# Kernel optimization log

Measured on AMD Instinct MI355X. Metric: run time of the kernel, lower is better.

Reference implementation:

```python
import jax, jax.numpy as jnp
import numpy as np

B, D_IN, D_HID, D_OUT = 32768, 512, 4096, 512
EPS = 1e-12  # F.normalize eps


def setup_inputs() -> dict:
    key = jax.random.key(0)
    ks = jax.random.split(key, 9)
    # Weights scaled up from the original 0.001 init so the norm_max clamp
    # branch is actually exercised (norms vary around the threshold).
    return {
        "x": jax.random.normal(ks[0], (B, D_IN), jnp.float32),
        "in_mean": jax.random.normal(ks[1], (D_IN,), jnp.float32) * 0.1,
        "in_std": jax.random.uniform(ks[2], (D_IN,), jnp.float32, 0.5, 1.5),
        "out_mean": jax.random.normal(ks[3], (D_OUT,), jnp.float32) * 0.1,
        "out_std": jax.random.uniform(ks[4], (D_OUT,), jnp.float32, 0.5, 1.5),
        "W1": jax.random.normal(ks[5], (D_HID, D_IN), jnp.float32) * 0.02,
        "b1": jax.random.normal(ks[6], (D_HID,), jnp.float32) * 0.001,
        "W2": jax.random.normal(ks[7], (D_OUT, D_HID), jnp.float32) * 0.02,
        "b2": jax.random.normal(ks[8], (D_OUT,), jnp.float32) * 0.001,
        "norm_max": 1,
    }


def reference(x, in_mean, in_std, out_mean, out_std, W1, b1, W2, b2, norm_max):
    norm_max = jnp.float32(norm_max)
    x_copy = x[..., :512]
    # input normalization
    xn = (x - in_mean) / in_std
    # 2-layer MLP: Linear -> ReLU -> Linear
    h = jax.nn.relu(jnp.einsum("bi,hi->bh", xn, W1) + b1)
    res = jnp.einsum("bh,oh->bo", h, W2) + b2
    # vectorized per-row norm clamp (torch loop: rescale rows with norm > norm_max)
    norms = jnp.linalg.norm(res, axis=-1, keepdims=True)  # [B,1]
    scale = norm_max / jax.lax.stop_gradient(norms)
    res = jnp.where(norms > norm_max, res * scale, res)
    # output de-normalization (torch subtracts norm_input[0] here)
    res = res * out_std + out_mean - in_mean
    # residual + L2 normalize
    mapped = res + x_copy
    mnorm = jnp.linalg.norm(mapped, axis=-1, keepdims=True)
    return mapped / jnp.maximum(mnorm, EPS)
```

## Files before the change

kernel.cpp:

```cpp
#include <hip/hip_runtime.h>
#include <hip/hip_bf16.h>

#define NB 32768
#define DIN 512
#define DHID 4096
#define DOUT 512

typedef __attribute__((ext_vector_type(8))) __bf16 bf16x8;
typedef __attribute__((ext_vector_type(4))) float f32x4;

__device__ __forceinline__ unsigned short f2bf(float f) {
  unsigned u = __builtin_bit_cast(unsigned, f);
  u += 0x7FFFu + ((u >> 16) & 1u);
  return (unsigned short)(u >> 16);
}

__device__ __forceinline__ void gload16(void* lds, const void* g) {
  __builtin_amdgcn_global_load_lds(
      (const __attribute__((address_space(1))) void*)g,
      (__attribute__((address_space(3))) void*)lds, 16, 0, 0);
}

__global__ __launch_bounds__(256) void k_prep_x(
    const float4* __restrict__ x, const float* __restrict__ mean,
    const float* __restrict__ stdv, ushort4* __restrict__ xn) {
  const int i = blockIdx.x * 256 + threadIdx.x;
  const int col = (i << 2) & (DIN - 1);
  const float4 v = x[i];
  const float4 m = *(const float4*)(mean + col);
  const float4 s = *(const float4*)(stdv + col);
  ushort4 o;
  o.x = f2bf((v.x - m.x) / s.x);
  o.y = f2bf((v.y - m.y) / s.y);
  o.z = f2bf((v.z - m.z) / s.z);
  o.w = f2bf((v.w - m.w) / s.w);
  xn[i] = o;
}

__global__ __launch_bounds__(256) void k_cvt(
    const float4* __restrict__ in, ushort4* __restrict__ out) {
  const int i = blockIdx.x * 256 + threadIdx.x;
  const float4 v = in[i];
  ushort4 o;
  o.x = f2bf(v.x); o.y = f2bf(v.y); o.z = f2bf(v.z); o.w = f2bf(v.w);
  out[i] = o;
}

__global__ __launch_bounds__(512, 2) void k_gemm1(
    const unsigned short* __restrict__ A, const unsigned short* __restrict__ W,
    const float* __restrict__ bias, unsigned short* __restrict__ outp,
    const int N, const int K, const int nbn) {
  __shared__ __align__(16) char lds[3 * 49152];
  const int tid = threadIdx.x;
  const int wave = tid >> 6, lane = tid & 63;
  const int wm = wave >> 1, wn = wave & 1;
  const int lidlo = lane & 15, lidhi = lane >> 4;

  const int nwg = (int)gridDim.x;
  const int wg = (int)blockIdx.x;
  const int q = nwg >> 3, r = nwg & 7;
  const int xcd = wg & 7, loc = wg >> 3;
  const int swz = (xcd < r ? xcd * (q + 1) : r * (q + 1) + (xcd - r) * q) + loc;
  const int bm = swz / nbn, bn = swz % nbn;
  const int R0 = bm * 256, C0 = bn * 128;

  const int NT = K >> 6;
  const int dbase0 = wave * 1024;

  auto STAGE = [&](int t, int s) {
    char* as = lds + s * 49152;
    char* bs = as + 32768;
    const int k0 = t << 6;
#pragma unroll
    for (int i = 0; i < 4; ++i) {
      const int db = i * 8192 + dbase0;
      const int d = db + lane * 16;
      const int row = d >> 7;
      const int colb = (d & 127) ^ ((row & 7) << 4);
      gload16(as + db,
              (const char*)A + ((size_t)(R0 + row) * K + k0) * 2 + colb);
    }
#pragma unroll
    for (int i = 0; i < 2; ++i) {
      const int db = i * 8192 + dbase0;
      const int d = db + lane * 16;
      const int row = d >> 7;
      const int colb = (d & 127) ^ ((row & 7) << 4);
      gload16(bs + db,
              (const char*)W + ((size_t)(C0 + row) * K + k0) * 2 + colb);
    }
  };

  f32x4 acc[4][4] = {};

  STAGE(0, 0);
  STAGE(1, 1);
  asm volatile("s_waitcnt vmcnt(6)" ::: "memory");
  __builtin_amdgcn_s_barrier();

  int slot = 0;
  for (int t = 0; t < NT; ++t) {
    const int nslot = (slot == 2) ? 0 : slot + 1;
    const int sslot = (nslot == 2) ? 0 : nslot + 1;
    if (t + 2 < NT) STAGE(t + 2, sslot);

    const char* as = lds + slot * 49152;
    const char* bs = as + 32768;
    bf16x8 af[2][4], bw[2][4];
#pragma unroll
    for (int kk = 0; kk < 2; ++kk) {
#pragma unroll
      for (int i = 0; i < 4; ++i) {
        const int ra = wm * 64 + i * 16 + lidlo;
        af[kk][i] = *(const bf16x8*)(
            as + ra * 128 + ((kk * 64 + lidhi * 16) ^ ((ra & 7) << 4)));
        const int rb = wn * 64 + i * 16 + lidlo;
        bw[kk][i] = *(const bf16x8*)(
            bs + rb * 128 + ((kk * 64 + lidhi * 16) ^ ((rb & 7) << 4)));
      }
    }
    __builtin_amdgcn_s_setprio(1);
#pragma unroll
    for (int kk = 0; kk < 2; ++kk)
#pragma unroll
      for (int i = 0; i < 4; ++i)
#pragma unroll
        for (int j = 0; j < 4; ++j)
          acc[i][j] = __builtin_amdgcn_mfma_f32_16x16x32_bf16(
              af[kk][i], bw[kk][j], acc[i][j], 0, 0, 0);
    __builtin_amdgcn_s_setprio(0);

    if (t + 2 < NT) {
      asm volatile("s_waitcnt vmcnt(6)" ::: "memory");
    } else {
      asm volatile("s_waitcnt vmcnt(0)" ::: "memory");
    }
    __builtin_amdgcn_s_barrier();
    slot = nslot;
  }

  const int m0 = R0 + wm * 64 + (lidhi << 2);
  const int n0 = C0 + wn * 64 + lidlo;
#pragma unroll
  for (int j = 0; j < 4; ++j) {
    const int n = n0 + j * 16;
    const float bv = bias[n];
#pragma unroll
    for (int i = 0; i < 4; ++i) {
#pragma unroll
      for (int rr = 0; rr < 4; ++rr) {
        const int m = m0 + i * 16 + rr;
        float v = fmaxf(acc[i][j][rr] + bv, 0.0f);
        outp[(size_t)m * N + n] = f2bf(v);
      }
    }
  }
}

__global__ __launch_bounds__(512, 2) void k_gemm2(
    const unsigned short* __restrict__ A, const unsigned short* __restrict__ W,
    const float* __restrict__ bias, const float* __restrict__ x,
    const float* __restrict__ out_mean, const float* __restrict__ out_std,
    const float* __restrict__ in_mean, const int* __restrict__ nmp,
    float* __restrict__ outp, const int K) {
  __shared__ __align__(16) char lds[2 * 81920];
  const int tid = threadIdx.x;
  const int wave = tid >> 6, lane = tid & 63;
  const int wm = wave >> 2, wn = wave & 3;
  const int lidlo = lane & 15, lidhi = lane >> 4;

  const int nwg = (int)gridDim.x;
  const int wg = (int)blockIdx.x;
  const int q = nwg >> 3, r = nwg & 7;
  const int xcd = wg & 7, loc = wg >> 3;
  const int bm = (xcd < r ? xcd * (q + 1) : r * (q + 1) + (xcd - r) * q) + loc;
  const int R0 = bm * 128;

  const int NT = K >> 6;

  auto STAGE = [&](int t, int s) {
    char* as = lds + s * 81920;
    char* bs = as + 16384;
    const int k0 = t << 6;
#pragma unroll
    for (int i = 0; i < 10; ++i) {
      const int c = wave * 10 + i;
      if (c < 16) {
        const int d = c * 1024 + lane * 16;
        const int row = d >> 7;
        const int colb = (d & 127) ^ ((row & 7) << 4);
        gload16(as + c * 1024,
                (const char*)A + ((size_t)(R0 + row) * K + k0) * 2 + colb);
      } else {
        const int d = (c - 16) * 1024 + lane * 16;
        const int row = d >> 7;
        const int colb = (d & 127) ^ ((row & 7) << 4);
        gload16(bs + (c - 16) * 1024,
                (const char*)W + ((size_t)row * K + k0) * 2 + colb);
      }
    }
  };

  f32x4 acc[4][8] = {};

  STAGE(0, 0);
  asm volatile("s_waitcnt vmcnt(0)" ::: "memory");
  __builtin_amdgcn_s_barrier();

  for (int t = 0; t < NT; ++t) {
    if (t + 1 < NT) STAGE(t + 1, (t + 1) & 1);
    const char* as = lds + (t & 1) * 81920;
    const char* bs = as + 16384;
#pragma unroll
    for (int kk = 0; kk < 2; ++kk) {
      bf16x8 af[4], bw[8];
#pragma unroll
      for (int i = 0; i < 4; ++i) {
        const int ra = wm * 64 + i * 16 + lidlo;
        af[i] = *(const bf16x8*)(
            as + ra * 128 + ((kk * 64 + lidhi * 16) ^ ((ra & 7) << 4)));
      }
#pragma unroll
      for (int j = 0; j < 8; ++j) {
        const int rb = wn * 128 + j * 16 + lidlo;
        bw[j] = *(const bf16x8*)(
            bs + rb * 128 + ((kk * 64 + lidhi * 16) ^ ((rb & 7) << 4)));
      }
      __builtin_amdgcn_s_setprio(1);
#pragma unroll
      for (int i = 0; i < 4; ++i)
#pragma unroll
        for (int j = 0; j < 8; ++j)
          acc[i][j] = __builtin_amdgcn_mfma_f32_16x16x32_bf16(
              af[i], bw[j], acc[i][j], 0, 0, 0);
      __builtin_amdgcn_s_setprio(0);
    }
    asm volatile("s_waitcnt vmcnt(0)" ::: "memory");
    __builtin_amdgcn_s_barrier();
  }

  float* red = (float*)lds;
  const int n0 = wn * 128 + lidlo;
  float bv[8], os[8], omim[8];
#pragma unroll
  for (int j = 0; j < 8; ++j) {
    const int n = n0 + j * 16;
    bv[j] = bias[n];
    os[j] = out_std[n];
    omim[j] = out_mean[n] - in_mean[n];
  }
  const float nm = (float)(*nmp);
  const int lmb = wm * 64 + (lidhi << 2);

  float scr[4][4];
#pragma unroll
  for (int i = 0; i < 4; ++i) {
#pragma unroll
    for (int rr = 0; rr < 4; ++rr) {
      float s = 0.0f;
#pragma unroll
      for (int j = 0; j < 8; ++j) {
        const float v = acc[i][j][rr] + bv[j];
        acc[i][j][rr] = v;
        s += v * v;
      }
      s += __shfl_xor(s, 1); s += __shfl_xor(s, 2);
      s += __shfl_xor(s, 4); s += __shfl_xor(s, 8);
      scr[i][rr] = s;
    }
  }
  if (lidlo == 0) {
#pragma unroll
    for (int i = 0; i < 4; ++i)
#pragma unroll
      for (int rr = 0; rr < 4; ++rr)
        red[wn * 128 + lmb + i * 16 + rr] = scr[i][rr];
  }
  __syncthreads();
#pragma unroll
  for (int i = 0; i < 4; ++i) {
#pragma unroll
    for (int rr = 0; rr < 4; ++rr) {
      const int lm = lmb + i * 16 + rr;
      const float t = red[lm] + red[128 + lm] + red[256 + lm] + red[384 + lm];
      const float rn = sqrtf(t);
      scr[i][rr] = (rn > nm) ? (nm / rn) : 1.0f;
    }
  }
  __syncthreads();

  float s2a[4][4];
#pragma unroll
  for (int i = 0; i < 4; ++i) {
#pragma unroll
    for (int rr = 0; rr < 4; ++rr) {
      const int row = R0 + lmb + i * 16 + rr;
      const float sc = scr[i][rr];
      float s = 0.0f;
#pragma unroll
      for (int j = 0; j < 8; ++j) {
        const int n = n0 + j * 16;
        const float mv = acc[i][j][rr] * sc * os[j] + omim[j] +
                         x[(size_t)row * DOUT + n];
        acc[i][j][rr] = mv;
        s += mv * mv;
      }
      s += __shfl_xor(s, 1); s += __shfl_xor(s, 2);
      s += __shfl_xor(s, 4); s += __shfl_xor(s, 8);
      s2a[i][rr] = s;
    }
  }
  if (lidlo == 0) {
#pragma unroll
    for (int i = 0; i < 4; ++i)
#pragma unroll
      for (int rr = 0; rr < 4; ++rr)
        red[wn * 128 + lmb + i * 16 + rr] = s2a[i][rr];
  }
  __syncthreads();
#pragma unroll
  for (int i = 0; i < 4; ++i) {
#pragma unroll
    for (int rr = 0; rr < 4; ++rr) {
      const int lm = lmb + i * 16 + rr;
      const float t = red[lm] + red[128 + lm] + red[256 + lm] + red[384 + lm];
      const float inv = 1.0f / fmaxf(sqrtf(t), 1e-12f);
      const int row = R0 + lm;
#pragma unroll
      for (int j = 0; j < 8; ++j) {
        const int n = n0 + j * 16;
        outp[(size_t)row * DOUT + n] = acc[i][j][rr] * inv;
      }
    }
  }
}

extern "C" void kernel_launch(void* const* d_in, const int* in_sizes, int n_in,
                              void* d_out, int out_size, void* d_ws, size_t ws_size,
                              hipStream_t stream) {
  const float* x = (const float*)d_in[0];
  const float* in_mean = (const float*)d_in[1];
  const float* in_std = (const float*)d_in[2];
  const float* out_mean = (const float*)d_in[3];
  const float* out_std = (const float*)d_in[4];
  const float* W1 = (const float*)d_in[5];
  const float* b1 = (const float*)d_in[6];
  const float* W2 = (const float*)d_in[7];
  const float* b2 = (const float*)d_in[8];
  const int* nmp = (const int*)d_in[9];
  float* out = (float*)d_out;

  char* ws = (char*)d_ws;
  unsigned short* xn = (unsigned short*)ws;   ws += (size_t)NB * DIN * 2;
  unsigned short* W1b = (unsigned short*)ws;  ws += (size_t)DHID * DIN * 2;
  unsigned short* W2b = (unsigned short*)ws;  ws += (size_t)DOUT * DHID * 2;
  unsigned short* h = (unsigned short*)ws;

  const size_t fixedB = (size_t)(ws - (char*)d_ws);
  const size_t avail = (ws_size > fixedB) ? (ws_size - fixedB) : 0;
  long long crows = (long long)(avail / ((size_t)DHID * 2));
  if (crows > NB) crows = NB;
  crows &= ~255LL;
  if (crows < 256) crows = 256;
  const int chunk = (int)crows;

  k_prep_x<<<16384, 256, 0, stream>>>((const float4*)x, in_mean, in_std,
                                      (ushort4*)xn);
  k_cvt<<<2048, 256, 0, stream>>>((const float4*)W1, (ushort4*)W1b);
  k_cvt<<<2048, 256, 0, stream>>>((const float4*)W2, (ushort4*)W2b);

  for (int s = 0; s < NB; s += chunk) {
    const int mc = (NB - s < chunk) ? (NB - s) : chunk;
    const int g1 = (mc / 256) * (DHID / 128);
    k_gemm1<<<g1, 512, 0, stream>>>(xn + (size_t)s * DIN, W1b, b1, h,
                                    DHID, DIN, DHID / 128);
    const int g2 = mc / 128;
    k_gemm2<<<g2, 512, 0, stream>>>(h, W2b, b2, x + (size_t)s * DIN,
                                    out_mean, out_std, in_mean, nmp,
                                    out + (size_t)s * DOUT, DHID);
  }
}
```

Baseline: 474.0 us.

## Split GEMM k-loop into two phases interleaving prefetch with LDS reads and MFMA

Splits each 64-wide k tile of the GEMM main loop into two half-phases. Each phase issues half of the next-next tile's global-to-LDS loads, reads its LDS fragments, synchronises with barriers and sched_barrier fences, then runs its 16 MFMAs. The goal is to spread global load issue across the MMA work, in the style of a ping-pong schedule, and to roughly halve fragment register pressure. In exchange it adds extra barriers per iteration and explicit lgkmcnt waits, which could cost more in synchronisation than the overlap gains.

```diff
diff --git a/kernel.cpp b/kernel.cpp
--- a/kernel.cpp
+++ b/kernel.cpp
@@ -67,34 +67,32 @@
   const int NT = K >> 6;
   const int dbase0 = wave * 1024;
 
-  auto STAGE = [&](int t, int s) {
+  auto STAGE1 = [&](int t, int s, int i) {
     char* as = lds + s * 49152;
-    char* bs = as + 32768;
     const int k0 = t << 6;
-#pragma unroll
-    for (int i = 0; i < 4; ++i) {
+    if (i < 4) {
       const int db = i * 8192 + dbase0;
       const int d = db + lane * 16;
       const int row = d >> 7;
       const int colb = (d & 127) ^ ((row & 7) << 4);
       gload16(as + db,
               (const char*)A + ((size_t)(R0 + row) * K + k0) * 2 + colb);
-    }
-#pragma unroll
-    for (int i = 0; i < 2; ++i) {
-      const int db = i * 8192 + dbase0;
+    } else {
+      const int db = (i - 4) * 8192 + dbase0;
       const int d = db + lane * 16;
       const int row = d >> 7;
       const int colb = (d & 127) ^ ((row & 7) << 4);
-      gload16(bs + db,
+      gload16(as + 32768 + db,
               (const char*)W + ((size_t)(C0 + row) * K + k0) * 2 + colb);
     }
   };
 
   f32x4 acc[4][4] = {};
 
-  STAGE(0, 0);
-  STAGE(1, 1);
+#pragma unroll
+  for (int i = 0; i < 6; ++i) STAGE1(0, 0, i);
+#pragma unroll
+  for (int i = 0; i < 6; ++i) STAGE1(1, 1, i);
   asm volatile("s_waitcnt vmcnt(6)" ::: "memory");
   __builtin_amdgcn_s_barrier();
 
@@ -102,40 +100,48 @@
   for (int t = 0; t < NT; ++t) {
     const int nslot = (slot == 2) ? 0 : slot + 1;
     const int sslot = (nslot == 2) ? 0 : nslot + 1;
-    if (t + 2 < NT) STAGE(t + 2, sslot);
-
     const char* as = lds + slot * 49152;
     const char* bs = as + 32768;
-    bf16x8 af[2][4], bw[2][4];
+    const bool pf = (t + 2 < NT);
+
 #pragma unroll
     for (int kk = 0; kk < 2; ++kk) {
+      bf16x8 af[4], bw[4];
 #pragma unroll
       for (int i = 0; i < 4; ++i) {
         const int ra = wm * 64 + i * 16 + lidlo;
-        af[kk][i] = *(const bf16x8*)(
+        af[i] = *(const bf16x8*)(
             as + ra * 128 + ((kk * 64 + lidhi * 16) ^ ((ra & 7) << 4)));
         const int rb = wn * 64 + i * 16 + lidlo;
-        bw[kk][i] = *(const bf16x8*)(
+        bw[i] = *(const bf16x8*)(
             bs + rb * 128 + ((kk * 64 + lidhi * 16) ^ ((rb & 7) << 4)));
       }
-    }
-    __builtin_amdgcn_s_setprio(1);
-#pragma unroll
-    for (int kk = 0; kk < 2; ++kk)
+      if (pf) {
+#pragma unroll
+        for (int i = 0; i < 3; ++i) STAGE1(t + 2, sslot, kk * 3 + i);
+      }
+      __builtin_amdgcn_sched_barrier(0);
+      if (kk == 1) {
+        if (pf) {
+          asm volatile("s_waitcnt vmcnt(6)" ::: "memory");
+        } else {
+          asm volatile("s_waitcnt vmcnt(0)" ::: "memory");
+        }
+      }
+      __builtin_amdgcn_s_barrier();
+      asm volatile("s_waitcnt lgkmcnt(0)" ::: "memory");
+      __builtin_amdgcn_sched_barrier(0);
+      __builtin_amdgcn_s_setprio(1);
 #pragma unroll
       for (int i = 0; i < 4; ++i)
 #pragma unroll
         for (int j = 0; j < 4; ++j)
           acc[i][j] = __builtin_amdgcn_mfma_f32_16x16x32_bf16(
-              af[kk][i], bw[kk][j], acc[i][j], 0, 0, 0);
-    __builtin_amdgcn_s_setprio(0);
-
-    if (t + 2 < NT) {
-      asm volatile("s_waitcnt vmcnt(6)" ::: "memory");
-    } else {
-      asm volatile("s_waitcnt vmcnt(0)" ::: "memory");
-    }
-    __builtin_amdgcn_s_barrier();
+              af[i], bw[j], acc[i][j], 0, 0, 0);
+      __builtin_amdgcn_s_setprio(0);
+      __builtin_amdgcn_sched_barrier(0);
+      __builtin_amdgcn_s_barrier();
+    }
     slot = nslot;
   }
 
```

Result: no change. 475.3 us (+0.3%).
